# Optimization experiments

Measured on AMD Instinct MI355X. Metric: run time of the kernel, lower is better.

Reference implementation:

```python
import jax, jax.numpy as jnp
import numpy as np

EPS = 1e-07
GAMMA = 2.0
LAMBDA_DISCO = 1000.0


def _binary_entropy(target, output):
    x = jnp.clip(output, EPS, 1.0 - EPS)
    return -target * jnp.log(x) - (1.0 - target) * jnp.log(1.0 - x)


def _focal_bce(target, output, y_class, y_pred_class):
    yc = y_class[:, 0]
    ypc = y_pred_class[:, 0]
    y_pred = output[:, 0]
    bce = _binary_entropy(target, y_pred)
    m = jnp.mean(ypc)
    s = jnp.std(ypc)  # population std, matches tf.math.reduce_std
    norm = jnp.clip((ypc - m) / (2.0 * s) + 0.5, 0.0, 1.0)
    class_weight_factor = ((1.0 - yc) * norm) ** GAMMA
    norm_factor = jnp.sum(1.0 - yc) / jnp.sum(class_weight_factor)
    return class_weight_factor * bce * norm_factor


def _distance_corr(var_1, var_2, w, power):
    # pairwise |x_i - x_j| distance matrices [N, N]
    amat = jnp.abs(var_1[:, None] - var_1[None, :])
    bmat = jnp.abs(var_2[:, None] - var_2[None, :])
    amatavg = jnp.mean(amat * w, axis=1)
    bmatavg = jnp.mean(bmat * w, axis=1)
    # double centering (tile layout: minuend_1[i,j]=avg[j], minuend_2[i,j]=avg[i])
    Amat = amat - amatavg[None, :] - amatavg[:, None] + jnp.mean(amatavg * w)
    Bmat = bmat - bmatavg[None, :] - bmatavg[:, None] + jnp.mean(bmatavg * w)
    ABavg = jnp.abs(jnp.mean(Amat * Bmat * w, axis=1))
    AAavg = jnp.mean(Amat * Amat * w, axis=1)
    BBavg = jnp.mean(Bmat * Bmat * w, axis=1)
    mAB = jnp.mean(ABavg * w)
    mAA = jnp.mean(AAavg * w)
    mBB = jnp.mean(BBavg * w)
    if power == 1:
        dCorr = mAB / jnp.sqrt(jnp.abs(mAA * mBB) + 1e-12)
    elif power == 2:
        dCorr = mAB ** 2 / (jnp.abs(mAA * mBB) + 1e-12)
    else:
        dCorr = (mAB / jnp.sqrt(mAA * mBB) + 1e-12) ** power
    dCorr = jnp.where(jnp.isnan(dCorr), 0.0, dCorr)
    dCorr = jnp.where(dCorr < 0.0, 0.0, dCorr)
    return dCorr


def setup_inputs() -> dict:
    N = 4096
    key = jax.random.key(0)
    ks = jax.random.split(key, 6)
    target = jnp.round(jax.random.uniform(ks[0], (N,), dtype=jnp.float32))
    output = jax.random.uniform(ks[1], (N, 1), dtype=jnp.float32, minval=0.02, maxval=0.98)
    y_class = jnp.round(jax.random.uniform(ks[2], (N, 1), dtype=jnp.float32))
    y_pred_class = jax.random.uniform(ks[3], (N, 1), dtype=jnp.float32, minval=0.02, maxval=0.98)
    var_1 = jax.random.normal(ks[4], (N,), dtype=jnp.float32) * 20.0 + 100.0  # mass-like
    var_2 = jax.random.uniform(ks[5], (N,), dtype=jnp.float32)  # classifier-output-like
    normedweight = jnp.ones((N,), dtype=jnp.float32)  # sums to N as required
    return {"target": target, "output": output, "y_class": y_class,
            "y_pred_class": y_pred_class, "var_1": var_1, "var_2": var_2,
            "normedweight": normedweight, "power": 1}


def reference(target, output, y_class, y_pred_class, var_1, var_2, normedweight, power):
    focal = _focal_bce(target, output, y_class, y_pred_class)
    dcorr = _distance_corr(var_1, var_2, normedweight, power)
    return jnp.mean(focal) + LAMBDA_DISCO * dcorr
```

## Files before the change

### kernel.cpp

```cpp
#include <hip/hip_runtime.h>
#include <math.h>

#define N 4096
#define TILE 256
#define NBLK_1D 16
#define FEPS 1e-7f


__device__ __forceinline__ double block_reduce(double v) {
    __shared__ double buf[4];
    int tid = threadIdx.x;
    #pragma unroll
    for (int o = 32; o > 0; o >>= 1) v += __shfl_down(v, o, 64);
    __syncthreads();
    if ((tid & 63) == 0) buf[tid >> 6] = v;
    __syncthreads();
    return buf[0] + buf[1] + buf[2] + buf[3];
}

__global__ __launch_bounds__(256) void k_focal(
        const float* __restrict__ target,
        const float* __restrict__ output,
        const float* __restrict__ y_class,
        const float* __restrict__ y_pred_class,
        double* __restrict__ wd,
        float* __restrict__ row_zero ) {
    int tid = threadIdx.x;

    for (int i = tid; i < 5 * N; i += 256) row_zero[i] = 0.0f;

    double s_ypc = 0.0, s_ypc2 = 0.0, s_yc = 0.0;
    for (int i = tid; i < N; i += 256) {
        float ypc = y_pred_class[i];
        s_ypc  += (double)ypc;
        s_ypc2 += (double)ypc * (double)ypc;
        s_yc   += (double)y_class[i];
    }
    double t_ypc  = block_reduce(s_ypc);
    double t_ypc2 = block_reduce(s_ypc2);
    double t_yc   = block_reduce(s_yc);

    __shared__ float  sm, sinv2s;
    __shared__ double s_sum1myc;
    if (tid == 0) {
        double m   = t_ypc / (double)N;
        double var = t_ypc2 / (double)N - m * m;
        double sd  = sqrt(var > 0.0 ? var : 0.0);
        sm     = (float)m;
        sinv2s = (float)(1.0 / (2.0 * sd));
        s_sum1myc = (double)N - t_yc;
    }
    __syncthreads();

    float m = sm, inv2s = sinv2s;
    double s_cwf = 0.0, s_cwfb = 0.0;
    for (int i = tid; i < N; i += 256) {
        float yc  = y_class[i];
        float ypc = y_pred_class[i];
        float nrm = (ypc - m) * inv2s + 0.5f;
        nrm = fminf(fmaxf(nrm, 0.0f), 1.0f);
        float c1  = (1.0f - yc) * nrm;
        float cwf = c1 * c1;
        float x = fminf(fmaxf(output[i], FEPS), 1.0f - FEPS);
        float t = target[i];
        float bce = -t * logf(x) - (1.0f - t) * logf(1.0f - x);
        s_cwf  += (double)cwf;
        s_cwfb += (double)cwf * (double)bce;
    }
    double t_cwf  = block_reduce(s_cwf);
    double t_cwfb = block_reduce(s_cwfb);
    if (tid == 0) {
        double norm_factor = s_sum1myc / t_cwf;
        wd[0] = t_cwfb * norm_factor / (double)N;
    }
}

__global__ __launch_bounds__(256) void k_pass1(
        const float* __restrict__ v1,
        const float* __restrict__ v2,
        const float* __restrict__ w,
        float* __restrict__ rowA,
        float* __restrict__ rowB) {
    __shared__ float s1[TILE], s2[TILE], sw[TILE];
    int tid = threadIdx.x;
    int bi = blockIdx.x & (NBLK_1D - 1);
    int bj = blockIdx.x >> 4;
    int j0 = bj * TILE;

    s1[tid] = v1[j0 + tid];
    s2[tid] = v2[j0 + tid];
    sw[tid] = w [j0 + tid];
    __syncthreads();

    int i = bi * TILE + tid;
    float a = v1[i];
    float b = v2[i];
    float sa = 0.0f, sb = 0.0f;
    #pragma unroll 16
    for (int j = 0; j < TILE; ++j) {
        sa = fmaf(fabsf(a - s1[j]), sw[j], sa);
        sb = fmaf(fabsf(b - s2[j]), sw[j], sb);
    }
    atomicAdd(&rowA[i], sa);
    atomicAdd(&rowB[i], sb);
}

__global__ __launch_bounds__(256) void k_pass2(
        const float* __restrict__ v1,
        const float* __restrict__ v2,
        const float* __restrict__ w,
        const float* __restrict__ rowA,
        const float* __restrict__ rowB,
        float* __restrict__ rowAB,
        float* __restrict__ rowAA,
        float* __restrict__ rowBB) {
    __shared__ float s1[TILE], s2[TILE], sw[TILE], sav[TILE], sbv[TILE];
    int tid = threadIdx.x;
    int bi = blockIdx.x & (NBLK_1D - 1);
    int bj = blockIdx.x >> 4;
    int j0 = bj * TILE;
    const float invN = 1.0f / (float)N;

    {
        int j = j0 + tid;
        s1[tid]  = v1[j];
        s2[tid]  = v2[j];
        sw[tid]  = w[j];
        sav[tid] = rowA[j] * invN;
        sbv[tid] = rowB[j] * invN;
    }
    __syncthreads();

    double sgA = 0.0, sgB = 0.0;
    for (int i = tid; i < N; i += 256) {
        double wi = (double)w[i];
        sgA += (double)rowA[i] * wi;
        sgB += (double)rowB[i] * wi;
    }
    const double NN = (double)N * (double)N;
    float gA = (float)(block_reduce(sgA) / NN);
    float gB = (float)(block_reduce(sgB) / NN);

    int i = bi * TILE + tid;
    float a = v1[i];
    float b = v2[i];
    float cA = rowA[i] * invN - gA;
    float cB = rowB[i] * invN - gB;

    float ab = 0.0f, aa = 0.0f, bb = 0.0f;
    #pragma unroll 8
    for (int j = 0; j < TILE; ++j) {
        float Am = fabsf(a - s1[j]) - sav[j] - cA;
        float Bm = fabsf(b - s2[j]) - sbv[j] - cB;
        float wj = sw[j];
        float Amw = Am * wj;
        float Bmw = Bm * wj;
        ab = fmaf(Amw, Bm, ab);
        aa = fmaf(Amw, Am, aa);
        bb = fmaf(Bmw, Bm, bb);
    }
    atomicAdd(&rowAB[i], ab);
    atomicAdd(&rowAA[i], aa);
    atomicAdd(&rowBB[i], bb);
}

__global__ __launch_bounds__(256) void k_final(
        const float* __restrict__ rowAB,
        const float* __restrict__ rowAA,
        const float* __restrict__ rowBB,
        const float* __restrict__ w,
        const double* __restrict__ wd,
        const int* __restrict__ power,
        float* __restrict__ out) {
    int tid = threadIdx.x;
    double sab = 0.0, saa = 0.0, sbb = 0.0;
    for (int i = tid; i < N; i += 256) {
        double wi = (double)w[i];
        sab += fabs((double)rowAB[i]) * wi;
        saa += (double)rowAA[i] * wi;
        sbb += (double)rowBB[i] * wi;
    }
    double tab = block_reduce(sab);
    double taa = block_reduce(saa);
    double tbb = block_reduce(sbb);
    if (tid == 0) {
        const double NN = (double)N * (double)N;
        double mAB = tab / NN;
        double mAA = taa / NN;
        double mBB = tbb / NN;
        int p = power[0];
        double d;
        if (p == 1) {
            d = mAB / sqrt(fabs(mAA * mBB) + 1e-12);
        } else if (p == 2) {
            d = (mAB * mAB) / (fabs(mAA * mBB) + 1e-12);
        } else {
            d = pow(mAB / sqrt(mAA * mBB) + 1e-12, (double)p);
        }
        if (isnan(d)) d = 0.0;
        if (d < 0.0)  d = 0.0;
        out[0] = (float)(wd[0] + 1000.0 * d);
    }
}

extern "C" void kernel_launch(void* const* d_in, const int* in_sizes, int n_in,
                              void* d_out, int out_size, void* d_ws, size_t ws_size,
                              hipStream_t stream) {
    const float* target       = (const float*)d_in[0];
    const float* output       = (const float*)d_in[1];
    const float* y_class      = (const float*)d_in[2];
    const float* y_pred_class = (const float*)d_in[3];
    const float* var_1        = (const float*)d_in[4];
    const float* var_2        = (const float*)d_in[5];
    const float* normedweight = (const float*)d_in[6];
    const int*   power        = (const int*)d_in[7];
    float* out = (float*)d_out;

    char*   ws    = (char*)d_ws;
    double* wd    = (double*)ws;
    float*  rowA  = (float*)(ws + 128);
    float*  rowB  = rowA  + N;
    float*  rowAB = rowB  + N;
    float*  rowAA = rowAB + N;
    float*  rowBB = rowAA + N;

    k_focal<<<1, 256, 0, stream>>>(target, output, y_class, y_pred_class, wd, rowA);
    k_pass1<<<NBLK_1D * NBLK_1D, 256, 0, stream>>>(var_1, var_2, normedweight, rowA, rowB);
    k_pass2<<<NBLK_1D * NBLK_1D, 256, 0, stream>>>(var_1, var_2, normedweight,
                                                   rowA, rowB, rowAB, rowAA, rowBB);
    k_final<<<1, 256, 0, stream>>>(rowAB, rowAA, rowBB, normedweight, wd, power, out);
}
```

Baseline: 43.39 us.

## Fuse four kernels into two with full-row blocks and last-block reduction

The four launches become two. The focal-loss block runs as an extra block of the first pass, and the final reduction folds into the second pass through an atomic counter, so the last block to finish does it. Each block now covers 16 full rows, with 16 lanes per row and float4 shared-memory reads. This removes the atomicAdd accumulation and the zeroing of the row buffers. The aim is to cut launch overhead and atomic traffic, in exchange for a larger shared-memory footprint and threadfence-based cross-block synchronisation.

```diff
diff --git a/kernel.cpp b/kernel.cpp
--- a/kernel.cpp
+++ b/kernel.cpp
@@ -2,8 +2,10 @@
 #include <math.h>
 
 #define N 4096
-#define TILE 256
-#define NBLK_1D 16
+#define RPB 16
+#define LANES 16
+#define NBLK (N / RPB)
+#define HALF 2048
 #define FEPS 1e-7f
 
 
@@ -18,118 +20,123 @@
     return buf[0] + buf[1] + buf[2] + buf[3];
 }
 
-__global__ __launch_bounds__(256) void k_focal(
+__global__ __launch_bounds__(256) void k1(
         const float* __restrict__ target,
         const float* __restrict__ output,
         const float* __restrict__ y_class,
         const float* __restrict__ y_pred_class,
-        double* __restrict__ wd,
-        float* __restrict__ row_zero ) {
-    int tid = threadIdx.x;
-
-    for (int i = tid; i < 5 * N; i += 256) row_zero[i] = 0.0f;
-
-    double s_ypc = 0.0, s_ypc2 = 0.0, s_yc = 0.0;
-    for (int i = tid; i < N; i += 256) {
-        float ypc = y_pred_class[i];
-        s_ypc  += (double)ypc;
-        s_ypc2 += (double)ypc * (double)ypc;
-        s_yc   += (double)y_class[i];
-    }
-    double t_ypc  = block_reduce(s_ypc);
-    double t_ypc2 = block_reduce(s_ypc2);
-    double t_yc   = block_reduce(s_yc);
-
-    __shared__ float  sm, sinv2s;
-    __shared__ double s_sum1myc;
-    if (tid == 0) {
-        double m   = t_ypc / (double)N;
-        double var = t_ypc2 / (double)N - m * m;
-        double sd  = sqrt(var > 0.0 ? var : 0.0);
-        sm     = (float)m;
-        sinv2s = (float)(1.0 / (2.0 * sd));
-        s_sum1myc = (double)N - t_yc;
-    }
-    __syncthreads();
-
-    float m = sm, inv2s = sinv2s;
-    double s_cwf = 0.0, s_cwfb = 0.0;
-    for (int i = tid; i < N; i += 256) {
-        float yc  = y_class[i];
-        float ypc = y_pred_class[i];
-        float nrm = (ypc - m) * inv2s + 0.5f;
-        nrm = fminf(fmaxf(nrm, 0.0f), 1.0f);
-        float c1  = (1.0f - yc) * nrm;
-        float cwf = c1 * c1;
-        float x = fminf(fmaxf(output[i], FEPS), 1.0f - FEPS);
-        float t = target[i];
-        float bce = -t * logf(x) - (1.0f - t) * logf(1.0f - x);
-        s_cwf  += (double)cwf;
-        s_cwfb += (double)cwf * (double)bce;
-    }
-    double t_cwf  = block_reduce(s_cwf);
-    double t_cwfb = block_reduce(s_cwfb);
-    if (tid == 0) {
-        double norm_factor = s_sum1myc / t_cwf;
-        wd[0] = t_cwfb * norm_factor / (double)N;
-    }
-}
-
-__global__ __launch_bounds__(256) void k_pass1(
         const float* __restrict__ v1,
         const float* __restrict__ v2,
         const float* __restrict__ w,
+        double* __restrict__ wd,
+        int* __restrict__ counter,
         float* __restrict__ rowA,
         float* __restrict__ rowB) {
-    __shared__ float s1[TILE], s2[TILE], sw[TILE];
     int tid = threadIdx.x;
-    int bi = blockIdx.x & (NBLK_1D - 1);
-    int bj = blockIdx.x >> 4;
-    int j0 = bj * TILE;
-
-    s1[tid] = v1[j0 + tid];
-    s2[tid] = v2[j0 + tid];
-    sw[tid] = w [j0 + tid];
-    __syncthreads();
-
-    int i = bi * TILE + tid;
-    float a = v1[i];
-    float b = v2[i];
+    int b = blockIdx.x;
+
+    if (b == NBLK) {
+        if (tid == 0) *counter = 0;
+        double s_ypc = 0.0, s_ypc2 = 0.0, s_yc = 0.0;
+        for (int i = tid; i < N; i += 256) {
+            float ypc = y_pred_class[i];
+            s_ypc  += (double)ypc;
+            s_ypc2 += (double)ypc * (double)ypc;
+            s_yc   += (double)y_class[i];
+        }
+        double t_ypc  = block_reduce(s_ypc);
+        double t_ypc2 = block_reduce(s_ypc2);
+        double t_yc   = block_reduce(s_yc);
+
+        __shared__ float  sm, sinv2s;
+        __shared__ double s_sum1myc;
+        if (tid == 0) {
+            double m   = t_ypc / (double)N;
+            double var = t_ypc2 / (double)N - m * m;
+            double sd  = sqrt(var > 0.0 ? var : 0.0);
+            sm     = (float)m;
+            sinv2s = (float)(1.0 / (2.0 * sd));
+            s_sum1myc = (double)N - t_yc;
+        }
+        __syncthreads();
+
+        float m = sm, inv2s = sinv2s;
+        double s_cwf = 0.0, s_cwfb = 0.0;
+        for (int i = tid; i < N; i += 256) {
+            float yc  = y_class[i];
+            float ypc = y_pred_class[i];
+            float nrm = (ypc - m) * inv2s + 0.5f;
+            nrm = fminf(fmaxf(nrm, 0.0f), 1.0f);
+            float c1  = (1.0f - yc) * nrm;
+            float cwf = c1 * c1;
+            float x = fminf(fmaxf(output[i], FEPS), 1.0f - FEPS);
+            float t = target[i];
+            float bce = -t * logf(x) - (1.0f - t) * logf(1.0f - x);
+            s_cwf  += (double)cwf;
+            s_cwfb += (double)cwf * (double)bce;
+        }
+        double t_cwf  = block_reduce(s_cwf);
+        double t_cwfb = block_reduce(s_cwfb);
+        if (tid == 0) wd[0] = t_cwfb * (s_sum1myc / t_cwf) / (double)N;
+        return;
+    }
+
+    __shared__ float s1[N], s2[N], sw[N];
+    #pragma unroll
+    for (int i = tid * 4; i < N; i += 1024) {
+        *(float4*)&s1[i] = *(const float4*)&v1[i];
+        *(float4*)&s2[i] = *(const float4*)&v2[i];
+        *(float4*)&sw[i] = *(const float4*)&w [i];
+    }
+    __syncthreads();
+
+    int lane16 = tid & (LANES - 1);
+    int r      = tid >> 4;
+    int i      = b * RPB + r;
+    float a  = s1[i];
+    float bb = s2[i];
     float sa = 0.0f, sb = 0.0f;
-    #pragma unroll 16
-    for (int j = 0; j < TILE; ++j) {
-        sa = fmaf(fabsf(a - s1[j]), sw[j], sa);
-        sb = fmaf(fabsf(b - s2[j]), sw[j], sb);
-    }
-    atomicAdd(&rowA[i], sa);
-    atomicAdd(&rowB[i], sb);
-}
-
-__global__ __launch_bounds__(256) void k_pass2(
+    #pragma unroll 8
+    for (int k = 0; k < N / (LANES * 4); ++k) {
+        int j = 4 * lane16 + 64 * k;
+        float4 x1 = *(const float4*)&s1[j];
+        float4 x2 = *(const float4*)&s2[j];
+        float4 xw = *(const float4*)&sw[j];
+        sa = fmaf(fabsf(a - x1.x), xw.x, sa);
+        sa = fmaf(fabsf(a - x1.y), xw.y, sa);
+        sa = fmaf(fabsf(a - x1.z), xw.z, sa);
+        sa = fmaf(fabsf(a - x1.w), xw.w, sa);
+        sb = fmaf(fabsf(bb - x2.x), xw.x, sb);
+        sb = fmaf(fabsf(bb - x2.y), xw.y, sb);
+        sb = fmaf(fabsf(bb - x2.z), xw.z, sb);
+        sb = fmaf(fabsf(bb - x2.w), xw.w, sb);
+    }
+    #pragma unroll
+    for (int o = 1; o < LANES; o <<= 1) {
+        sa += __shfl_xor(sa, o, LANES);
+        sb += __shfl_xor(sb, o, LANES);
+    }
+    if (lane16 == 0) { rowA[i] = sa; rowB[i] = sb; }
+}
+
+__global__ __launch_bounds__(256) void k2(
         const float* __restrict__ v1,
         const float* __restrict__ v2,
         const float* __restrict__ w,
         const float* __restrict__ rowA,
         const float* __restrict__ rowB,
-        float* __restrict__ rowAB,
-        float* __restrict__ rowAA,
-        float* __restrict__ rowBB) {
-    __shared__ float s1[TILE], s2[TILE], sw[TILE], sav[TILE], sbv[TILE];
+        const double* __restrict__ wd,
+        const int* __restrict__ power,
+        int* __restrict__ counter,
+        double* __restrict__ pAB,
+        double* __restrict__ pAA,
+        double* __restrict__ pBB,
+        float* __restrict__ out) {
+    __shared__ float s1[HALF], s2[HALF], sw[HALF], sav[HALF], sbv[HALF];
+    __shared__ double rAB[RPB], rAA[RPB], rBB[RPB];
     int tid = threadIdx.x;
-    int bi = blockIdx.x & (NBLK_1D - 1);
-    int bj = blockIdx.x >> 4;
-    int j0 = bj * TILE;
+    int b = blockIdx.x;
     const float invN = 1.0f / (float)N;
-
-    {
-        int j = j0 + tid;
-        s1[tid]  = v1[j];
-        s2[tid]  = v2[j];
-        sw[tid]  = w[j];
-        sav[tid] = rowA[j] * invN;
-        sbv[tid] = rowB[j] * invN;
-    }
-    __syncthreads();
 
     double sgA = 0.0, sgB = 0.0;
     for (int i = tid; i < N; i += 256) {
@@ -141,53 +148,91 @@
     float gA = (float)(block_reduce(sgA) / NN);
     float gB = (float)(block_reduce(sgB) / NN);
 
-    int i = bi * TILE + tid;
-    float a = v1[i];
-    float b = v2[i];
+    int lane16 = tid & (LANES - 1);
+    int r      = tid >> 4;
+    int i      = b * RPB + r;
+    float a  = v1[i];
+    float bb = v2[i];
     float cA = rowA[i] * invN - gA;
     float cB = rowB[i] * invN - gB;
 
-    float ab = 0.0f, aa = 0.0f, bb = 0.0f;
-    #pragma unroll 8
-    for (int j = 0; j < TILE; ++j) {
-        float Am = fabsf(a - s1[j]) - sav[j] - cA;
-        float Bm = fabsf(b - s2[j]) - sbv[j] - cB;
-        float wj = sw[j];
-        float Amw = Am * wj;
-        float Bmw = Bm * wj;
-        ab = fmaf(Amw, Bm, ab);
-        aa = fmaf(Amw, Am, aa);
-        bb = fmaf(Bmw, Bm, bb);
-    }
-    atomicAdd(&rowAB[i], ab);
-    atomicAdd(&rowAA[i], aa);
-    atomicAdd(&rowBB[i], bb);
-}
-
-__global__ __launch_bounds__(256) void k_final(
-        const float* __restrict__ rowAB,
-        const float* __restrict__ rowAA,
-        const float* __restrict__ rowBB,
-        const float* __restrict__ w,
-        const double* __restrict__ wd,
-        const int* __restrict__ power,
-        float* __restrict__ out) {
-    int tid = threadIdx.x;
-    double sab = 0.0, saa = 0.0, sbb = 0.0;
-    for (int i = tid; i < N; i += 256) {
+    float ab = 0.0f, aa = 0.0f, bbs = 0.0f;
+    for (int h = 0; h < 2; ++h) {
+        int j0 = h * HALF;
+        __syncthreads();
+        #pragma unroll
+        for (int t = tid * 4; t < HALF; t += 1024) {
+            *(float4*)&s1[t] = *(const float4*)&v1[j0 + t];
+            *(float4*)&s2[t] = *(const float4*)&v2[j0 + t];
+            *(float4*)&sw[t] = *(const float4*)&w [j0 + t];
+            float4 ra = *(const float4*)&rowA[j0 + t];
+            float4 rb = *(const float4*)&rowB[j0 + t];
+            ra.x *= invN; ra.y *= invN; ra.z *= invN; ra.w *= invN;
+            rb.x *= invN; rb.y *= invN; rb.z *= invN; rb.w *= invN;
+            *(float4*)&sav[t] = ra;
+            *(float4*)&sbv[t] = rb;
+        }
+        __syncthreads();
+        #pragma unroll 4
+        for (int k = 0; k < HALF / (LANES * 4); ++k) {
+            int j = 4 * lane16 + 64 * k;
+            float4 x1 = *(const float4*)&s1[j];
+            float4 x2 = *(const float4*)&s2[j];
+            float4 xw = *(const float4*)&sw[j];
+            float4 xa = *(const float4*)&sav[j];
+            float4 xb = *(const float4*)&sbv[j];
+            #define STEP(c)                                              \
+            {                                                            \
+                float Am = fabsf(a  - x1.c) - xa.c - cA;                 \
+                float Bm = fabsf(bb - x2.c) - xb.c - cB;                 \
+                float Amw = Am * xw.c;                                   \
+                ab  = fmaf(Amw, Bm, ab);                                 \
+                aa  = fmaf(Amw, Am, aa);                                 \
+                bbs = fmaf(Bm * xw.c, Bm, bbs);                          \
+            }
+            STEP(x) STEP(y) STEP(z) STEP(w)
+            #undef STEP
+        }
+    }
+    #pragma unroll
+    for (int o = 1; o < LANES; o <<= 1) {
+        ab  += __shfl_xor(ab,  o, LANES);
+        aa  += __shfl_xor(aa,  o, LANES);
+        bbs += __shfl_xor(bbs, o, LANES);
+    }
+    if (lane16 == 0) {
         double wi = (double)w[i];
-        sab += fabs((double)rowAB[i]) * wi;
-        saa += (double)rowAA[i] * wi;
-        sbb += (double)rowBB[i] * wi;
-    }
-    double tab = block_reduce(sab);
-    double taa = block_reduce(saa);
-    double tbb = block_reduce(sbb);
+        rAB[r] = fabs((double)ab) * wi;
+        rAA[r] = (double)aa * wi;
+        rBB[r] = (double)bbs * wi;
+    }
+    __syncthreads();
     if (tid == 0) {
-        const double NN = (double)N * (double)N;
-        double mAB = tab / NN;
-        double mAA = taa / NN;
-        double mBB = tbb / NN;
+        double tab = 0.0, taa = 0.0, tbb = 0.0;
+        #pragma unroll
+        for (int q = 0; q < RPB; ++q) { tab += rAB[q]; taa += rAA[q]; tbb += rBB[q]; }
+        pAB[b] = tab; pAA[b] = taa; pBB[b] = tbb;
+    }
+
+    __shared__ int isLast;
+    if (tid == 0) {
+        __threadfence();
+        int old = atomicAdd(counter, 1);
+        isLast = (old == NBLK - 1);
+    }
+    __syncthreads();
+    if (!isLast) return;
+    __threadfence();
+
+    double vab = pAB[tid], vaa = pAA[tid], vbb = pBB[tid];
+    double tab = block_reduce(vab);
+    double taa = block_reduce(vaa);
+    double tbb = block_reduce(vbb);
+    if (tid == 0) {
+        const double NN2 = (double)N * (double)N;
+        double mAB = tab / NN2;
+        double mAA = taa / NN2;
+        double mBB = tbb / NN2;
         int p = power[0];
         double d;
         if (p == 1) {
@@ -216,17 +261,17 @@
     const int*   power        = (const int*)d_in[7];
     float* out = (float*)d_out;
 
-    char*   ws    = (char*)d_ws;
-    double* wd    = (double*)ws;
-    float*  rowA  = (float*)(ws + 128);
-    float*  rowB  = rowA  + N;
-    float*  rowAB = rowB  + N;
-    float*  rowAA = rowAB + N;
-    float*  rowBB = rowAA + N;
-
-    k_focal<<<1, 256, 0, stream>>>(target, output, y_class, y_pred_class, wd, rowA);
-    k_pass1<<<NBLK_1D * NBLK_1D, 256, 0, stream>>>(var_1, var_2, normedweight, rowA, rowB);
-    k_pass2<<<NBLK_1D * NBLK_1D, 256, 0, stream>>>(var_1, var_2, normedweight,
-                                                   rowA, rowB, rowAB, rowAA, rowBB);
-    k_final<<<1, 256, 0, stream>>>(rowAB, rowAA, rowBB, normedweight, wd, power, out);
-}
+    char*   ws      = (char*)d_ws;
+    double* wd      = (double*)ws;
+    int*    counter = (int*)(ws + 16);
+    double* pAB     = (double*)(ws + 64);
+    double* pAA     = pAB + NBLK;
+    double* pBB     = pAA + NBLK;
+    float*  rowA    = (float*)(pBB + NBLK);
+    float*  rowB    = rowA + N;
+
+    k1<<<NBLK + 1, 256, 0, stream>>>(target, output, y_class, y_pred_class,
+                                     var_1, var_2, normedweight, wd, counter, rowA, rowB);
+    k2<<<NBLK, 256, 0, stream>>>(var_1, var_2, normedweight, rowA, rowB,
+                                 wd, power, counter, pAB, pAA, pBB, out);
+}
```

Measured after the change: 37.03 us. 1.17x faster.
